# Kernel optimization log

Hardware: AMD Instinct MI355X
Metric: run time of the kernel (lower is better)

## Reference

```python
import jax, jax.numpy as jnp
import numpy as np

H = 16        # num_attention_heads
E = 1024      # hidden_size
D = E // H    # attention_head_size = 64
M = 1024      # max_position_embeddings
EPS = 1e-12


def setup_inputs() -> dict:
    key = jax.random.key(0)
    ks = jax.random.split(key, 12)
    s = 0.02
    B, S = 8, 1024
    return {
        "hidden_states": jax.random.normal(ks[0], (B, S, E), jnp.float32),
        "Wq": jax.random.normal(ks[1], (E, E), jnp.float32) * s,
        "bq": jnp.zeros((E,), jnp.float32),
        "Wk": jax.random.normal(ks[2], (E, E), jnp.float32) * s,
        "bk": jnp.zeros((E,), jnp.float32),
        "Wv": jax.random.normal(ks[3], (E, E), jnp.float32) * s,
        "bv": jnp.zeros((E,), jnp.float32),
        "dist_emb": jax.random.normal(ks[4], (2 * M - 1, D), jnp.float32) * s,
        "Wo": jax.random.normal(ks[5], (E, E), jnp.float32) * s,
        "bo": jnp.zeros((E,), jnp.float32),
        "ln_gamma": jnp.ones((E,), jnp.float32),
        "ln_beta": jnp.zeros((E,), jnp.float32),
    }


def reference(hidden_states, Wq, bq, Wk, bk, Wv, bv, dist_emb, Wo, bo, ln_gamma, ln_beta):
    B, S, _ = hidden_states.shape

    def heads(x):  # [B,S,E] -> [B,H,S,D]
        return x.reshape(B, S, H, D).transpose(0, 2, 1, 3)

    q = heads(hidden_states @ Wq + bq)
    k = heads(hidden_states @ Wk + bk)
    v = heads(hidden_states @ Wv + bv)

    scores = jnp.einsum("bhqd,bhkd->bhqk", q, k)

    # relative_key_query positional bias
    pos_l = jnp.arange(S)[:, None]
    pos_r = jnp.arange(S)[None, :]
    dist_idx = pos_l - pos_r + M - 1            # [S,S] in [0, 2M-2]
    pos_emb = dist_emb[dist_idx]                # [S,S,D]  (l, r, d)
    rel_q = jnp.einsum("bhld,lrd->bhlr", q, pos_emb)
    rel_k = jnp.einsum("bhrd,lrd->bhlr", k, pos_emb)
    scores = (scores + rel_q + rel_k) / jnp.sqrt(jnp.asarray(D, scores.dtype))

    probs = jax.nn.softmax(scores, axis=-1)     # dropout prob = 0 (eval)
    ctx = jnp.einsum("bhqk,bhkd->bhqd", probs, v)
    ctx = ctx.transpose(0, 2, 1, 3).reshape(B, S, E)

    # BertSelfOutput: dense + residual + LayerNorm
    h = ctx @ Wo + bo + hidden_states
    mu = jnp.mean(h, axis=-1, keepdims=True)
    var = jnp.mean(jnp.square(h - mu), axis=-1, keepdims=True)
    out = (h - mu) * jax.lax.rsqrt(var + EPS) * ln_gamma + ln_beta
    return out
```

## Files before the change

### kernel.cpp

```cpp
#include <hip/hip_runtime.h>


typedef unsigned short u16;
typedef unsigned int u32;
typedef unsigned long long u64;
typedef __bf16 bf16x8 __attribute__((ext_vector_type(8)));
typedef float  f32x4  __attribute__((ext_vector_type(4)));
typedef int    i32x4  __attribute__((ext_vector_type(4)));

__device__ __forceinline__ float b2f(u16 u) {
  union { u32 i; float f; } x;
  x.i = ((u32)u) << 16;
  return x.f;
}
__device__ __forceinline__ u16 f2b_manual(float f) {
  union { float f; u32 u; } x;
  x.f = f;
  return (u16)((x.u + 0x7FFFu + ((x.u >> 16) & 1u)) >> 16);
}
#if __has_builtin(__builtin_amdgcn_cvt_pk_bf16_f32)
typedef __bf16 bf16x2 __attribute__((ext_vector_type(2)));
__device__ __forceinline__ u32 cvt2(float a, float b) {
  union { bf16x2 v; u32 u; } x;
  x.v = __builtin_amdgcn_cvt_pk_bf16_f32(a, b);
  return x.u;
}
#else
__device__ __forceinline__ u32 cvt2(float a, float b) {
  return (u32)f2b_manual(a) | ((u32)f2b_manual(b) << 16);
}
#endif
__device__ __forceinline__ u16 f2b(float f) { return (u16)(cvt2(f, f) & 0xffffu); }

union LdU { i32x4 i4; bf16x8 b8; };
__device__ __forceinline__ bf16x8 ldb8(const u16* p) {
  LdU u; u.i4 = *(const i32x4*)p; return u.b8;
}
__device__ __forceinline__ void pack8(u16* dst, const float* src) {
  f32x4 lo = *(const f32x4*)src, hi = *(const f32x4*)(src + 4);
  i32x4 v;
  v.x = (int)cvt2(lo.x, lo.y); v.y = (int)cvt2(lo.z, lo.w);
  v.z = (int)cvt2(hi.x, hi.y); v.w = (int)cvt2(hi.z, hi.w);
  *(i32x4*)dst = v;
}
#define MFMA16(a, b, c) __builtin_amdgcn_mfma_f32_16x16x32_bf16((a), (b), (c), 0, 0, 0)

template <int C>
__device__ __forceinline__ float dppmov(float x) {
  union { float f; int i; } a, r;
  a.f = x;
  r.i = __builtin_amdgcn_update_dpp(0, a.i, C, 0xF, 0xF, true);
  return r.f;
}
__device__ __forceinline__ float rsum16(float x) {
  x += dppmov<0xB1>(x);
  x += dppmov<0x4E>(x);
  x += dppmov<0x141>(x);
  x += dppmov<0x140>(x);
  return x;
}
__device__ __forceinline__ float fexp2(float x) {
#if __has_builtin(__builtin_amdgcn_exp2f)
  return __builtin_amdgcn_exp2f(x);
#else
  return exp2f(x);
#endif
}

#if __has_builtin(__builtin_amdgcn_global_load_lds)
#define HAS_GLDS 1
typedef __attribute__((address_space(3))) u32 as3_u32;
typedef const __attribute__((address_space(1))) u32 as1_u32;
__device__ __forceinline__ void gld16(const u16* g, u16* lds_wave_base) {
  __builtin_amdgcn_global_load_lds(
      (as1_u32*)g, (as3_u32*)(u32)(u64)lds_wave_base, 16, 0, 0);
}
#else
#define HAS_GLDS 0
__device__ __forceinline__ void gld16_fb(const u16* g, u16* lds_wave_base,
                                         int lane) {
  *(i32x4*)(lds_wave_base + lane * 8) = *(const i32x4*)g;
}
#endif

#define SQRT_C2 0.42466090f

__global__ __launch_bounds__(256) void convX(
    const float* __restrict__ X, u16* __restrict__ Xb) {
  int i = (blockIdx.x * 256 + threadIdx.x) * 8;
  pack8(&Xb[i], &X[i]);
}

__global__ __launch_bounds__(256) void convD(
    const float* __restrict__ dist, u16* __restrict__ distb) {
  int i = (blockIdx.x * 256 + threadIdx.x) * 8;
  if (i < 2047 * 64) {
    float t[8];
#pragma unroll
    for (int j = 0; j < 8; j++) t[j] = dist[i + j] * SQRT_C2;
    pack8(&distb[i], t);
  }
}

__global__ __launch_bounds__(256) void convWt(
    const float* __restrict__ W, u16* __restrict__ Wt) {
  __shared__ float tile[64][65];
  const int tid = threadIdx.x;
  const int k0 = blockIdx.x * 64, m0 = blockIdx.y * 64;
#pragma unroll
  for (int it = 0; it < 4; it++) {
    int row = (tid >> 4) + 16 * it;
    int col = (tid & 15) * 4;
    f32x4 v = *(const f32x4*)&W[(size_t)(k0 + row) * 1024 + m0 + col];
    tile[row][col] = v.x; tile[row][col + 1] = v.y;
    tile[row][col + 2] = v.z; tile[row][col + 3] = v.w;
  }
  __syncthreads();
#pragma unroll
  for (int it = 0; it < 4; it++) {
    int mr = (tid >> 4) + 16 * it;
    int kc = (tid & 15) * 4;
    u32 w0 = cvt2(tile[kc][mr], tile[kc + 1][mr]);
    u32 w1 = cvt2(tile[kc + 2][mr], tile[kc + 3][mr]);
    *(u64*)&Wt[(size_t)(m0 + mr) * 1024 + k0 + kc] = (u64)w0 | ((u64)w1 << 32);
  }
}

__global__ __launch_bounds__(256) void transV(
    const u16* __restrict__ V, u16* __restrict__ Vt) {
  __shared__ u16 tile[64][72];
  const int tid = threadIdx.x;
  const int bh = blockIdx.y, b = bh >> 4, h = bh & 15;
  const int s0 = blockIdx.x << 6;
  const u16* Vb = V + (size_t)(b * 1024) * 1024 + h * 64;
  {
    int rp = tid >> 3, a = tid & 7;
    const u16* src = &Vb[(size_t)(s0 + 2 * rp) * 1024 + a * 8];
    i32x4 va = *(const i32x4*)src;
    i32x4 vb2 = *(const i32x4*)(src + 1024);
    u16 ta[8] __attribute__((aligned(16)));
    u16 tb[8] __attribute__((aligned(16)));
    *(i32x4*)ta = va; *(i32x4*)tb = vb2;
    int colb = ((((rp >> 2) ^ a) << 3) | ((2 * rp) & 7));
#pragma unroll
    for (int j = 0; j < 8; j++)
      *(u32*)&tile[a * 8 + j][colb] = (u32)ta[j] | ((u32)tb[j] << 16);
  }
  __syncthreads();
  int d = tid >> 2, cc = tid & 3;
  int sw = (d >> 3) & 7;
  i32x4 lo = *(const i32x4*)&tile[d][((2 * cc) ^ sw) << 3];
  i32x4 hi = *(const i32x4*)&tile[d][((2 * cc + 1) ^ sw) << 3];
  u16* dst = Vt + ((size_t)bh * 64 + d) * 1024 + s0 + cc * 16;
  *(i32x4*)dst = lo;
  *(i32x4*)(dst + 8) = hi;
}

template <int RESID, int OUTF32>
__global__ __launch_bounds__(256) void gemm_bb(
    const u16* __restrict__ A, const u16* __restrict__ Wt,
    const float* __restrict__ bias, const float* __restrict__ resid,
    float* __restrict__ outF, u16* __restrict__ outB, int N, int K, int M,
    float oscale) {
  __shared__ u16 sA[128 * 64];
  __shared__ u16 sW[128 * 64];

  const int tid = threadIdx.x;
  const int lane = tid & 63, w = tid >> 6;
  const int quad = lane >> 4, lb = lane & 15;
  const int m0 = blockIdx.x * 128, n0 = blockIdx.y * 128;

  const int srow = lane >> 3;
  const int gcol = ((lane & 7) ^ srow) << 3;

  f32x4 acc[2][8] = {};

  for (int k0 = 0; k0 < K; k0 += 64) {
#pragma unroll
    for (int j = 0; j < 4; j++) {
      int rb = (4 * w + j) * 8;
      const u16* ga = &A[(size_t)(n0 + rb + srow) * K + k0 + gcol];
      const u16* gw = &Wt[(size_t)(m0 + rb + srow) * K + k0 + gcol];
#if HAS_GLDS
      gld16(ga, &sA[rb * 64]);
      gld16(gw, &sW[rb * 64]);
#else
      gld16_fb(ga, &sA[rb * 64], lane);
      gld16_fb(gw, &sW[rb * 64], lane);
#endif
    }
    __syncthreads();

    const int r0 = 32 * w + lb;
    const int sw0 = r0 & 7;
    bf16x8 a00 = ldb8(&sA[r0 * 64 + ((quad ^ sw0) << 3)]);
    bf16x8 a01 = ldb8(&sA[r0 * 64 + (((4 + quad) ^ sw0) << 3)]);
    bf16x8 a10 = ldb8(&sA[(r0 + 16) * 64 + ((quad ^ sw0) << 3)]);
    bf16x8 a11 = ldb8(&sA[(r0 + 16) * 64 + (((4 + quad) ^ sw0) << 3)]);
#pragma unroll
    for (int t = 0; t < 8; t++) {
      int n = 16 * t + lb;
      int swn = n & 7;
      bf16x8 b0 = ldb8(&sW[n * 64 + ((quad ^ swn) << 3)]);
      bf16x8 b1 = ldb8(&sW[n * 64 + (((4 + quad) ^ swn) << 3)]);
      acc[0][t] = MFMA16(a00, b0, acc[0][t]);
      acc[0][t] = MFMA16(a01, b1, acc[0][t]);
      acc[1][t] = MFMA16(a10, b0, acc[1][t]);
      acc[1][t] = MFMA16(a11, b1, acc[1][t]);
    }
    __syncthreads();
  }

#pragma unroll
  for (int half = 0; half < 2; half++)
#pragma unroll
    for (int t = 0; t < 8; t++) {
      int col = m0 + 16 * t + lb;
      float bv = bias[col];
#pragma unroll
      for (int i = 0; i < 4; i++) {
        int rowg = n0 + 32 * w + 16 * half + quad * 4 + i;
        float v = acc[half][t][i] + bv;
        if (RESID) v += resid[(size_t)rowg * M + col];
        v *= oscale;
        if (OUTF32) outF[(size_t)rowg * M + col] = v;
        else        outB[(size_t)rowg * M + col] = f2b(v);
      }
    }
}

__global__ __launch_bounds__(256) void attn(
    const u16* __restrict__ Q, const u16* __restrict__ Kv,
    const u16* __restrict__ Vt, const u16* __restrict__ distb,
    u16* __restrict__ ctx) {
  __shared__ u16 sQ[64][72];
  __shared__ u16 sK[64][72];
  __shared__ u16 sVt[64][72];
  __shared__ u16 sP[128][72];
  __shared__ u16 sGq[128 * 64];
  __shared__ u16 sGk[128 * 64];

  const int tid = threadIdx.x;
  const int lane = tid & 63, w = tid >> 6;
  const int quad = lane >> 4, lb = lane & 15;
  const int bh = blockIdx.y, b = bh >> 4, h = bh & 15;
  const int q0 = blockIdx.x << 6;
  const int S = 1024, E = 1024;
  const u16* Qb = Q  + (size_t)(b * S) * E + h * 64;
  const u16* Kb = Kv + (size_t)(b * S) * E + h * 64;
  const u16* Vtb = Vt + (size_t)bh * 64 * 1024;

  const int sr = tid >> 3, sc8 = (tid & 7) << 3;

  {
    *(i32x4*)&sQ[sr][sc8] = *(const i32x4*)&Qb[(size_t)(q0 + sr) * E + sc8];
    *(i32x4*)&sQ[sr + 32][sc8] =
        *(const i32x4*)&Qb[(size_t)(q0 + sr + 32) * E + sc8];
    *(i32x4*)&sK[sr][sc8] = *(const i32x4*)&Kb[(size_t)sr * E + sc8];
    *(i32x4*)&sK[sr + 32][sc8] =
        *(const i32x4*)&Kb[(size_t)(sr + 32) * E + sc8];
    *(i32x4*)&sVt[sr][sc8] = *(const i32x4*)&Vtb[(size_t)sr * 1024 + sc8];
    *(i32x4*)&sVt[sr + 32][sc8] =
        *(const i32x4*)&Vtb[(size_t)(sr + 32) * 1024 + sc8];
    const int dbase = q0 + 960;
#pragma unroll
    for (int j = 0; j < 4; j++) {
      int p = sr + 32 * j;
      int g = dbase + p;
      if (g > 2046) g = 2046;
      *(i32x4*)&sP[p][sc8] = *(const i32x4*)&distb[(size_t)g * 64 + sc8];
    }
  }
  __syncthreads();

  const int row = 16 * w + lb;
  bf16x8 aq0 = ldb8(&sQ[row][quad * 8]);
  bf16x8 aq1 = ldb8(&sQ[row][32 + quad * 8]);

  const u16* kb  = &sK[lb][quad * 8];
  const u16* vbp = &sVt[lb][quad * 8];
  const u16* akb = &sK[row][quad * 8];
  const u16* pb  = &sP[lb][quad * 8];
  u16* gqsb = &sGq[lb * 64 + ((16 * w + 4 * quad) ^ ((lb & 7) << 3))];
  u16* gksb = &sGk[lb * 64 + ((16 * w + 4 * quad) ^ ((lb & 7) << 3))];
  u16* psb  = &sK[16 * w + 4 * quad][lb];
  const int rl_ = 16 * w + 4 * quad;
  const u16* gqa_[4];
  const u16* gka_[4][4];
#pragma unroll
  for (int i = 0; i < 4; i++) {
    int rl = rl_ + i;
    int c3 = rl - lb + 15;
    int sw8 = (c3 & 7) << 3;
    gqa_[i] = &sGq[(c3 << 6) + (rl ^ sw8)];
#pragma unroll
    for (int t = 0; t < 4; t++) {
      int c = rl - (16 * t + lb) + 63;
      gka_[i][t] = &sGk[(c << 6) + ((16 * t + lb) ^ sw8)];
    }
  }
  const u16* kg0 = Kb + (size_t)(64 + sr) * E + sc8;
  const u16* kg1 = kg0 + (size_t)32 * E;
  const u16* vg0 = Vtb + (size_t)sr * 1024 + 64 + sc8;
  const u16* vg1 = vg0 + (size_t)32 * 1024;
  const u16* dg0 = distb + (size_t)(q0 - 64 + 960 + sr) * 64 + sc8;
  const u16* dg1 = dg0 + (size_t)32 * 64;
  u16* wk0 = &sK[sr][sc8];  u16* wk1 = &sK[sr + 32][sc8];
  u16* wv0 = &sVt[sr][sc8]; u16* wv1 = &sVt[sr + 32][sc8];
  u16* wp0 = &sP[sr][sc8];  u16* wp1 = &sP[sr + 32][sc8];

  const int uqlo = w, uqhi = w + 4;
  const int uklo = 3 - w, ukhi = 7 - w;

  f32x4 accO[4] = {};
  float l_i[4] = {0.f, 0.f, 0.f, 0.f};

  for (int kt = 0; kt < 16; kt++) {
    const int xorv = (kt & 1) << 6;

    i32x4 kr0, kr1, vr0, vr1, dr0, dr1;
    if (kt < 15) {
      kr0 = *(const i32x4*)kg0;
      kr1 = *(const i32x4*)kg1;
      vr0 = *(const i32x4*)vg0;
      vr1 = *(const i32x4*)vg1;
      dr0 = *(const i32x4*)dg0;
      dr1 = *(const i32x4*)dg1;
    }

    __builtin_amdgcn_s_setprio(1);
    f32x4 accS[4] = {};
#pragma unroll
    for (int t = 0; t < 4; t++) {
      bf16x8 b0 = ldb8(kb + 1152 * t);
      bf16x8 b1 = ldb8(kb + 1152 * t + 32);
      accS[t] = MFMA16(aq0, b0, accS[t]);
      accS[t] = MFMA16(aq1, b1, accS[t]);
    }
    bf16x8 ak0 = ldb8(akb);
    bf16x8 ak1 = ldb8(akb + 32);
    const u16* pbA = pb + (xorv ? 4608 : 0);
    const u16* pbB = pb + (xorv ? -4608 : 0);
#pragma unroll
    for (int u = 0; u < 8; u++) {
      const bool doq = (u >= uqlo) && (u <= uqhi);
      const bool dok = (u >= uklo) && (u <= ukhi);
      if (doq || dok) {
        const u16* pp = (u < 4 ? pbA : pbB) + 1152 * u;
        bf16x8 p0 = ldb8(pp);
        bf16x8 p1 = ldb8(pp + 32);
        if (doq) {
          f32x4 gq = {};
          gq = MFMA16(aq0, p0, gq);
          gq = MFMA16(aq1, p1, gq);
          *(u32*)(gqsb + 1024 * u) = cvt2(gq[0], gq[1]);
          *(u32*)(gqsb + 1024 * u + 2) = cvt2(gq[2], gq[3]);
        }
        if (dok) {
          f32x4 gk = {};
          gk = MFMA16(ak0, p0, gk);
          gk = MFMA16(ak1, p1, gk);
          *(u32*)(gksb + 1024 * u) = cvt2(gk[0], gk[1]);
          *(u32*)(gksb + 1024 * u + 2) = cvt2(gk[2], gk[3]);
        }
      }
    }
    __builtin_amdgcn_s_setprio(0);
    __syncthreads();

    float pr[4][4];
#pragma unroll
    for (int t = 0; t < 4; t++) {
#pragma unroll
      for (int i = 0; i < 4; i++) {
        float s = accS[t][i] + b2f(gqa_[i][1024 * (3 - t)]) +
                  b2f(*gka_[i][t]);
        float e = fexp2(s);
        pr[t][i] = e;
        l_i[i] += e;
      }
    }

#pragma unroll
    for (int t = 0; t < 4; t++)
#pragma unroll
      for (int i = 0; i < 4; i++)
        psb[72 * i + 16 * t] = f2b(pr[t][i]);

    bf16x8 ap0 = ldb8(akb);
    bf16x8 ap1 = ldb8(akb + 32);
    __builtin_amdgcn_s_setprio(1);
#pragma unroll
    for (int t = 0; t < 4; t++) {
      bf16x8 v0 = ldb8(vbp + 1152 * t);
      bf16x8 v1 = ldb8(vbp + 1152 * t + 32);
      accO[t] = MFMA16(ap0, v0, accO[t]);
      accO[t] = MFMA16(ap1, v1, accO[t]);
    }
    __builtin_amdgcn_s_setprio(0);
    __syncthreads();

    if (kt < 15) {
      const int pxn = ((kt + 1) & 1) ? 4608 : 0;
      *(i32x4*)wk0 = kr0;
      *(i32x4*)wk1 = kr1;
      *(i32x4*)wv0 = vr0;
      *(i32x4*)wv1 = vr1;
      *(i32x4*)(wp0 + pxn) = dr0;
      *(i32x4*)(wp1 + pxn) = dr1;
      kg0 += (size_t)64 * E; kg1 += (size_t)64 * E;
      vg0 += 64;             vg1 += 64;
      dg0 -= 64 * 64;        dg1 -= 64 * 64;
      __syncthreads();
    }
  }

#pragma unroll
  for (int i = 0; i < 4; i++) l_i[i] = rsum16(l_i[i]);

  u16* Cb = ctx + (size_t)(b * S) * E + h * 64;
#pragma unroll
  for (int t = 0; t < 4; t++)
#pragma unroll
    for (int i = 0; i < 4; i++) {
      int rl = 16 * w + quad * 4 + i;
      Cb[(size_t)(q0 + rl) * E + 16 * t + lb] = f2b(accO[t][i] / l_i[i]);
    }
}

__global__ __launch_bounds__(256) void lnorm(
    const float* __restrict__ Hp, const float* __restrict__ gamma,
    const float* __restrict__ beta, float* __restrict__ out) {
  __shared__ float red[8];
  const int rowb = blockIdx.x, tid = threadIdx.x;
  const float* hr = Hp + (size_t)rowb * 1024;
  f32x4 v = *(const f32x4*)&hr[tid * 4];
  float s = v.x + v.y + v.z + v.w;
  float q = v.x * v.x + v.y * v.y + v.z * v.z + v.w * v.w;
#pragma unroll
  for (int d = 1; d < 64; d <<= 1) {
    s += __shfl_xor(s, d, 64);
    q += __shfl_xor(q, d, 64);
  }
  int w = tid >> 6, lane = tid & 63;
  if (lane == 0) { red[w] = s; red[4 + w] = q; }
  __syncthreads();
  s = red[0] + red[1] + red[2] + red[3];
  q = red[4] + red[5] + red[6] + red[7];
  float mu = s * (1.f / 1024.f);
  float var = q * (1.f / 1024.f) - mu * mu;
  float rstd = rsqrtf(var + 1e-12f);
  float* orow = out + (size_t)rowb * 1024;
  f32x4 o;
#pragma unroll
  for (int j = 0; j < 4; j++) {
    int c = tid * 4 + j;
    o[j] = (v[j] - mu) * rstd * gamma[c] + beta[c];
  }
  *(f32x4*)&orow[tid * 4] = o;
}

extern "C" void kernel_launch(void* const* d_in, const int* in_sizes, int n_in,
                              void* d_out, int out_size, void* d_ws,
                              size_t ws_size, hipStream_t stream) {
  const float* X    = (const float*)d_in[0];
  const float* Wq   = (const float*)d_in[1];
  const float* bq   = (const float*)d_in[2];
  const float* Wk   = (const float*)d_in[3];
  const float* bk   = (const float*)d_in[4];
  const float* Wv   = (const float*)d_in[5];
  const float* bv   = (const float*)d_in[6];
  const float* dist = (const float*)d_in[7];
  const float* Wo   = (const float*)d_in[8];
  const float* bo   = (const float*)d_in[9];
  const float* gam  = (const float*)d_in[10];
  const float* bet  = (const float*)d_in[11];

  const size_t NE = (size_t)8192 * 1024;
  char* ws = (char*)d_ws;
  u16* Qw = (u16*)(ws);
  u16* Kw = (u16*)(ws + 2 * NE);
  u16* Vw = (u16*)(ws + 4 * NE);
  u16* Cw = (u16*)(ws + 6 * NE);
  float* Hp = (float*)ws;

  char* ob = (char*)d_out;
  u16* Wtq = (u16*)(ob);
  u16* Wtk = (u16*)(ob + (2u << 20));
  u16* Wtv = (u16*)(ob + (4u << 20));
  u16* Wto = (u16*)(ob + (6u << 20));
  u16* Xb  = (u16*)(ob + (8u << 20));
  u16* Vtg = (u16*)(ob + (8u << 20));
  u16* distb = (u16*)(ob + (26u << 20));

  dim3 bb(256);
  dim3 gw(16, 16);
  convWt<<<gw, bb, 0, stream>>>(Wq, Wtq);
  convWt<<<gw, bb, 0, stream>>>(Wk, Wtk);
  convWt<<<gw, bb, 0, stream>>>(Wv, Wtv);
  convWt<<<gw, bb, 0, stream>>>(Wo, Wto);
  convX<<<dim3(4096), bb, 0, stream>>>(X, Xb);
  convD<<<dim3(64), bb, 0, stream>>>(dist, distb);

  dim3 gg(8, 64);
  gemm_bb<0, 0><<<gg, bb, 0, stream>>>(Xb, Wtq, bq, nullptr, nullptr, Qw, 8192, 1024, 1024, SQRT_C2);
  gemm_bb<0, 0><<<gg, bb, 0, stream>>>(Xb, Wtk, bk, nullptr, nullptr, Kw, 8192, 1024, 1024, SQRT_C2);
  gemm_bb<0, 0><<<gg, bb, 0, stream>>>(Xb, Wtv, bv, nullptr, nullptr, Vw, 8192, 1024, 1024, 1.0f);
  transV<<<dim3(16, 128), bb, 0, stream>>>(Vw, Vtg);
  attn<<<dim3(16, 128), bb, 0, stream>>>(Qw, Kw, Vtg, distb, Cw);
  gemm_bb<1, 1><<<gg, bb, 0, stream>>>(Cw, Wto, bo, X, Hp, nullptr, 8192, 1024, 1024, 1.0f);
  lnorm<<<dim3(8192), bb, 0, stream>>>(Hp, gam, bet, (float*)d_out);
}
```

Baseline: 431.2 us.

## Fuse QKV projections into one GEMM, remap attention blocks per XCD, repad K tile

The three Q/K/V projection GEMMs become one launch over a concatenated 3072-wide weight, with per-segment output pointers and scales and a concatenated bias copied into scratch. The GEMM grid is swapped so the M-tile index runs along blockIdx.x. Attention blocks are remapped so that all query tiles of a given batch-head land on the same XCD, which should improve L2 reuse of K/V. The sK/sP row pad changes from 72 to 76 to alter the LDS bank pattern. The fused GEMM relies on Wtq/Wtk/Wtv sitting contiguously in memory, and the new bias buffer lives in the output region.

```diff
diff --git a/kernel.cpp b/kernel.cpp
--- a/kernel.cpp
+++ b/kernel.cpp
@@ -156,7 +156,7 @@
   *(i32x4*)(dst + 8) = hi;
 }
 
-template <int RESID, int OUTF32>
+template <int RESID, int OUTF32, int QKV>
 __global__ __launch_bounds__(256) void gemm_bb(
     const u16* __restrict__ A, const u16* __restrict__ Wt,
     const float* __restrict__ bias, const float* __restrict__ resid,
@@ -168,7 +168,7 @@
   const int tid = threadIdx.x;
   const int lane = tid & 63, w = tid >> 6;
   const int quad = lane >> 4, lb = lane & 15;
-  const int m0 = blockIdx.x * 128, n0 = blockIdx.y * 128;
+  const int m0 = blockIdx.y * 128, n0 = blockIdx.x * 128;
 
   const int srow = lane >> 3;
   const int gcol = ((lane & 7) ^ srow) << 3;
@@ -211,20 +211,30 @@
     __syncthreads();
   }
 
+  u16* outSeg = outB;
+  float osc = oscale;
+  int mbase = m0;
+  if (QKV) {
+    outSeg = outB + (size_t)(m0 >> 10) * ((size_t)8192 * 1024);
+    osc = (m0 < 2048) ? SQRT_C2 : 1.0f;
+    mbase = m0 & 1023;
+  }
+
 #pragma unroll
   for (int half = 0; half < 2; half++)
 #pragma unroll
     for (int t = 0; t < 8; t++) {
       int col = m0 + 16 * t + lb;
+      int colw = mbase + 16 * t + lb;
       float bv = bias[col];
 #pragma unroll
       for (int i = 0; i < 4; i++) {
         int rowg = n0 + 32 * w + 16 * half + quad * 4 + i;
         float v = acc[half][t][i] + bv;
         if (RESID) v += resid[(size_t)rowg * M + col];
-        v *= oscale;
+        v *= osc;
         if (OUTF32) outF[(size_t)rowg * M + col] = v;
-        else        outB[(size_t)rowg * M + col] = f2b(v);
+        else        outSeg[(size_t)rowg * (QKV ? 1024 : M) + colw] = f2b(v);
       }
     }
 }
@@ -234,7 +244,7 @@
     const u16* __restrict__ Vt, const u16* __restrict__ distb,
     u16* __restrict__ ctx) {
   __shared__ u16 sQ[64][72];
-  __shared__ u16 sK[64][72];
+  __shared__ u16 sK[64][76];
   __shared__ u16 sVt[64][72];
   __shared__ u16 sP[128][72];
   __shared__ u16 sGq[128 * 64];
@@ -243,8 +253,11 @@
   const int tid = threadIdx.x;
   const int lane = tid & 63, w = tid >> 6;
   const int quad = lane >> 4, lb = lane & 15;
-  const int bh = blockIdx.y, b = bh >> 4, h = bh & 15;
-  const int q0 = blockIdx.x << 6;
+  const int f = blockIdx.y * 16 + blockIdx.x;
+  const int xcd = f & 7, slot = f >> 3;
+  const int bh = (xcd << 4) | (slot & 15);
+  const int q0 = (slot >> 4) << 6;
+  const int b = bh >> 4, h = bh & 15;
   const int S = 1024, E = 1024;
   const u16* Qb = Q  + (size_t)(b * S) * E + h * 64;
   const u16* Kb = Kv + (size_t)(b * S) * E + h * 64;
@@ -332,8 +345,8 @@
     f32x4 accS[4] = {};
 #pragma unroll
     for (int t = 0; t < 4; t++) {
-      bf16x8 b0 = ldb8(kb + 1152 * t);
-      bf16x8 b1 = ldb8(kb + 1152 * t + 32);
+      bf16x8 b0 = ldb8(kb + 1216 * t);
+      bf16x8 b1 = ldb8(kb + 1216 * t + 32);
       accS[t] = MFMA16(aq0, b0, accS[t]);
       accS[t] = MFMA16(aq1, b1, accS[t]);
     }
@@ -385,7 +398,7 @@
     for (int t = 0; t < 4; t++)
 #pragma unroll
       for (int i = 0; i < 4; i++)
-        psb[72 * i + 16 * t] = f2b(pr[t][i]);
+        psb[76 * i + 16 * t] = f2b(pr[t][i]);
 
     bf16x8 ap0 = ldb8(akb);
     bf16x8 ap1 = ldb8(akb + 32);
@@ -492,6 +505,7 @@
   u16* Xb  = (u16*)(ob + (8u << 20));
   u16* Vtg = (u16*)(ob + (8u << 20));
   u16* distb = (u16*)(ob + (26u << 20));
+  float* bias3 = (float*)(ob + (30u << 20));
 
   dim3 bb(256);
   dim3 gw(16, 16);
@@ -501,13 +515,15 @@
   convWt<<<gw, bb, 0, stream>>>(Wo, Wto);
   convX<<<dim3(4096), bb, 0, stream>>>(X, Xb);
   convD<<<dim3(64), bb, 0, stream>>>(dist, distb);
-
-  dim3 gg(8, 64);
-  gemm_bb<0, 0><<<gg, bb, 0, stream>>>(Xb, Wtq, bq, nullptr, nullptr, Qw, 8192, 1024, 1024, SQRT_C2);
-  gemm_bb<0, 0><<<gg, bb, 0, stream>>>(Xb, Wtk, bk, nullptr, nullptr, Kw, 8192, 1024, 1024, SQRT_C2);
-  gemm_bb<0, 0><<<gg, bb, 0, stream>>>(Xb, Wtv, bv, nullptr, nullptr, Vw, 8192, 1024, 1024, 1.0f);
+  hipMemcpyAsync(bias3, bq, 4096, hipMemcpyDeviceToDevice, stream);
+  hipMemcpyAsync(bias3 + 1024, bk, 4096, hipMemcpyDeviceToDevice, stream);
+  hipMemcpyAsync(bias3 + 2048, bv, 4096, hipMemcpyDeviceToDevice, stream);
+
+  gemm_bb<0, 0, 1><<<dim3(64, 24), bb, 0, stream>>>(
+      Xb, Wtq, bias3, nullptr, nullptr, Qw, 8192, 1024, 3072, 1.0f);
   transV<<<dim3(16, 128), bb, 0, stream>>>(Vw, Vtg);
   attn<<<dim3(16, 128), bb, 0, stream>>>(Qw, Kw, Vtg, distb, Cw);
-  gemm_bb<1, 1><<<gg, bb, 0, stream>>>(Cw, Wto, bo, X, Hp, nullptr, 8192, 1024, 1024, 1.0f);
+  gemm_bb<1, 1, 0><<<dim3(64, 8), bb, 0, stream>>>(
+      Cw, Wto, bo, X, Hp, nullptr, 8192, 1024, 1024, 1.0f);
   lnorm<<<dim3(8192), bb, 0, stream>>>(Hp, gam, bet, (float*)d_out);
 }
```

After: 567.0 us. +31.5%, slower.
